# Optimization experiments

Hardware: AMD Instinct MI355X
Metric: run time of the kernel (lower is better)

Reference implementation:

```python
import jax, jax.numpy as jnp
import numpy as np

D_MODEL = 512
NUM_HEADS = 8
D_K = D_MODEL // NUM_HEADS  # 64, also d_v
SEQ_LEN = 4096


def setup_inputs() -> dict:
    key = jax.random.key(0)
    k1, k2, k3, k4, k5 = jax.random.split(key, 5)
    scale = jnp.float32(1.0 / np.sqrt(D_MODEL))  # keep exp(scores) finite
    return {
        "embeded_seq": jax.random.normal(k1, (SEQ_LEN, D_MODEL), jnp.float32),
        "q_proj": jax.random.normal(k2, (NUM_HEADS, D_MODEL, D_K), jnp.float32) * scale,
        "k_proj": jax.random.normal(k3, (NUM_HEADS, D_MODEL, D_K), jnp.float32) * scale,
        "v_proj": jax.random.normal(k4, (NUM_HEADS, D_MODEL, D_K), jnp.float32) * scale,
        "out_proj": jax.random.normal(k5, (NUM_HEADS * D_K, D_MODEL), jnp.float32) * scale,
    }


def reference(embeded_seq, q_proj, k_proj, v_proj, out_proj):
    # Per-head linear projections: (S, D) x (H, D, d_k) -> (H, S, d_k)
    qs = jnp.einsum("sd,hdk->hsk", embeded_seq, q_proj)
    ks = jnp.einsum("sd,hdk->hsk", embeded_seq, k_proj)
    vs = jnp.einsum("sd,hdv->hsv", embeded_seq, v_proj)

    # Scores: (H, S, S), scaled by sqrt(d_k)
    scores = jnp.einsum("hsk,htk->hst", qs, ks) / jnp.float32(np.sqrt(D_K))

    # Faithful to the original: torch.sum(e_powered) is a GLOBAL scalar sum
    # over all heads and positions (a buggy "softmax"), not a row softmax.
    e = jnp.exp(scores)
    softmaxed = e / jnp.sum(e)

    # Attention output per head: (H, S, d_v)
    head_attns = jnp.einsum("hst,htv->hsv", softmaxed, vs)

    # Concat heads along feature dim -> (S, H*d_v), then output projection
    concat = jnp.transpose(head_attns, (1, 0, 2)).reshape(SEQ_LEN, NUM_HEADS * D_K)
    return concat @ out_proj
```

## Files before the change

kernel.cpp:

```cpp
#include <hip/hip_runtime.h>
#include <stdint.h>

#define S_LEN 4096
#define DMODEL 512
#define NHEAD 8
#define DK 64
#define SPLIT 4
#define TBLK 64
#define NT ((S_LEN / SPLIT) / TBLK)

typedef __attribute__((ext_vector_type(8))) short short8;
typedef __attribute__((ext_vector_type(4))) float f32x4;
typedef __attribute__((ext_vector_type(16))) float f32x16;
typedef __attribute__((ext_vector_type(4))) unsigned int uint4v;
typedef __attribute__((ext_vector_type(2))) unsigned long long ull2;

__device__ __forceinline__ unsigned short f2bf(float f) {
    unsigned int u = __float_as_uint(f);
    u = (u + 0x7fffu + ((u >> 16) & 1u)) >> 16;
    return (unsigned short)u;
}

__device__ __forceinline__ void gload16(const unsigned short* g, unsigned short* l) {
    __builtin_amdgcn_global_load_lds(
        (const __attribute__((address_space(1))) unsigned int*)g,
        (__attribute__((address_space(3))) unsigned int*)l, 16, 0, 0);
}


__global__ void cast_bf16_kernel(const float* __restrict__ in,
                                 unsigned short* __restrict__ out, int n4,
                                 float* __restrict__ Z) {
    int i = blockIdx.x * blockDim.x + threadIdx.x;
    if (i == 0) *Z = 0.0f;
    if (i >= n4) return;
    float4 v = reinterpret_cast<const float4*>(in)[i];
    ushort4 o;
    o.x = f2bf(v.x); o.y = f2bf(v.y); o.z = f2bf(v.z); o.w = f2bf(v.w);
    reinterpret_cast<ushort4*>(out)[i] = o;
}

__global__ __launch_bounds__(256) void transpose_qkv_kernel(
    const float* __restrict__ wq, const float* __restrict__ wk, const float* __restrict__ wv,
    unsigned short* __restrict__ oq, unsigned short* __restrict__ ok, unsigned short* __restrict__ ov) {
    __shared__ float tile[64][65];
    const int p = blockIdx.y >> 3, h = blockIdx.y & 7;
    const int r0 = blockIdx.x * 64;
    const float* in = ((p == 0) ? wq : (p == 1) ? wk : wv) + (size_t)h * DMODEL * DK;
    unsigned short* out = ((p == 0) ? oq : (p == 1) ? ok : ov) + (size_t)h * DK * DMODEL;
    const int tr = threadIdx.x >> 4, tc4 = (threadIdx.x & 15) * 4;
#pragma unroll
    for (int rr = 0; rr < 4; ++rr) {
        float4 v = *reinterpret_cast<const float4*>(in + (size_t)(r0 + tr + rr * 16) * DK + tc4);
        tile[tr + rr * 16][tc4 + 0] = v.x;
        tile[tr + rr * 16][tc4 + 1] = v.y;
        tile[tr + rr * 16][tc4 + 2] = v.z;
        tile[tr + rr * 16][tc4 + 3] = v.w;
    }
    __syncthreads();
#pragma unroll
    for (int rr = 0; rr < 4; ++rr) {
        const int c = tr + rr * 16;
        ushort4 o;
        o.x = f2bf(tile[tc4 + 0][c]);
        o.y = f2bf(tile[tc4 + 1][c]);
        o.z = f2bf(tile[tc4 + 2][c]);
        o.w = f2bf(tile[tc4 + 3][c]);
        *reinterpret_cast<ushort4*>(out + (size_t)c * DMODEL + r0 + tc4) = o;
    }
}

__global__ __launch_bounds__(256) void transpose_wo_kernel(
    const float* __restrict__ in, unsigned short* __restrict__ out) {
    __shared__ float tile[64][65];
    const int c0 = blockIdx.x * 64, r0 = blockIdx.y * 64;
    const int tr = threadIdx.x >> 4, tc4 = (threadIdx.x & 15) * 4;
#pragma unroll
    for (int rr = 0; rr < 4; ++rr) {
        float4 v = *reinterpret_cast<const float4*>(in + (size_t)(r0 + tr + rr * 16) * DMODEL + c0 + tc4);
        tile[tr + rr * 16][tc4 + 0] = v.x;
        tile[tr + rr * 16][tc4 + 1] = v.y;
        tile[tr + rr * 16][tc4 + 2] = v.z;
        tile[tr + rr * 16][tc4 + 3] = v.w;
    }
    __syncthreads();
#pragma unroll
    for (int rr = 0; rr < 4; ++rr) {
        const int c = tr + rr * 16;
        ushort4 o;
        o.x = f2bf(tile[tc4 + 0][c]);
        o.y = f2bf(tile[tc4 + 1][c]);
        o.z = f2bf(tile[tc4 + 2][c]);
        o.w = f2bf(tile[tc4 + 3][c]);
        *reinterpret_cast<ushort4*>(out + (size_t)(c0 + c) * DMODEL + r0 + tc4) = o;
    }
}

__global__ __launch_bounds__(256, 2) void proj_tiled_kernel(
    const unsigned short* __restrict__ A,
    const unsigned short* __restrict__ BTall,
    unsigned short* __restrict__ Qo,
    unsigned short* __restrict__ Ko,
    unsigned short* __restrict__ Vo) {
    __shared__ unsigned short lds[32768];
    const int tid = threadIdx.x;
    const int w = tid >> 6, l = tid & 63;
    const int l15 = l & 15, lg = l >> 4;
    const int wr = w >> 1, wc = w & 1;
    const int m0 = blockIdx.x * 128, n0 = blockIdx.y * 128;
    const int srow = l >> 3;
    const int schk = ((l & 7) ^ srow) << 3;
    f32x4 acc[4][4] = {};
    {
        unsigned short* ab = &lds[0];
        unsigned short* bb = &lds[8192];
#pragma unroll
        for (int g = 0; g < 4; ++g) {
            gload16(A + (size_t)(m0 + w * 32 + g * 8 + srow) * DMODEL + schk,
                    ab + (w * 32 + g * 8) * 64);
            gload16(BTall + (size_t)(n0 + w * 32 + g * 8 + srow) * DMODEL + schk,
                    bb + (w * 32 + g * 8) * 64);
        }
    }
    __syncthreads();
    for (int kt = 0; kt < 8; ++kt) {
        const int b = (kt & 1) * 16384;
        if (kt + 1 < 8) {
            const int nb = ((kt + 1) & 1) * 16384;
            const int k0 = (kt + 1) * 64;
            unsigned short* ab = &lds[nb];
            unsigned short* bb = &lds[nb + 8192];
#pragma unroll
            for (int g = 0; g < 4; ++g) {
                gload16(A + (size_t)(m0 + w * 32 + g * 8 + srow) * DMODEL + k0 + schk,
                        ab + (w * 32 + g * 8) * 64);
                gload16(BTall + (size_t)(n0 + w * 32 + g * 8 + srow) * DMODEL + k0 + schk,
                        bb + (w * 32 + g * 8) * 64);
            }
        }
#pragma unroll
        for (int kk = 0; kk < 2; ++kk) {
            short8 am[4], bn[4];
#pragma unroll
            for (int mi = 0; mi < 4; ++mi) {
                const int row = wr * 64 + mi * 16 + l15;
                am[mi] = *reinterpret_cast<const short8*>(
                    &lds[b + row * 64 + ((kk * 32 + lg * 8) ^ ((row & 7) << 3))]);
            }
#pragma unroll
            for (int ni = 0; ni < 4; ++ni) {
                const int row = wc * 64 + ni * 16 + l15;
                bn[ni] = *reinterpret_cast<const short8*>(
                    &lds[b + 8192 + row * 64 + ((kk * 32 + lg * 8) ^ ((row & 7) << 3))]);
            }
#pragma unroll
            for (int mi = 0; mi < 4; ++mi)
#pragma unroll
                for (int ni = 0; ni < 4; ++ni)
                    acc[mi][ni] = __builtin_amdgcn_mfma_f32_16x16x32_bf16(am[mi], bn[ni], acc[mi][ni], 0, 0, 0);
        }
        __syncthreads();
    }
#pragma unroll
    for (int ni = 0; ni < 4; ++ni) {
        const int n = n0 + wc * 64 + ni * 16;
        const int p = n >> 9, h = (n >> 6) & 7, vb = n & 63;
        unsigned short* dst = ((p == 0) ? Qo : (p == 1) ? Ko : Vo) + (size_t)h * S_LEN * DK;
        const float sc = (p == 0) ? 0.125f : 1.0f;
#pragma unroll
        for (int mi = 0; mi < 4; ++mi) {
            const int s = m0 + wr * 64 + mi * 16 + lg * 4;
#pragma unroll
            for (int r = 0; r < 4; ++r)
                dst[(size_t)(s + r) * DK + vb + l15] = f2bf(acc[mi][ni][r] * sc);
        }
    }
}

__global__ __launch_bounds__(256, 2) void out_tiled_kernel(
    const unsigned short* __restrict__ A,
    const unsigned short* __restrict__ BT,
    const float* __restrict__ Z,
    float* __restrict__ Cout) {
    __shared__ unsigned short lds[32768];
    const int tid = threadIdx.x;
    const int w = tid >> 6, l = tid & 63;
    const int l15 = l & 15, lg = l >> 4;
    const int wr = w >> 1, wc = w & 1;
    const int m0 = blockIdx.x * 128, n0 = blockIdx.y * 128;
    const int srow = l >> 3;
    const int schk = ((l & 7) ^ srow) << 3;
    const float invZ = 1.0f / *Z;
    f32x4 acc[4][4] = {};
    {
        unsigned short* ab = &lds[0];
        unsigned short* bb = &lds[8192];
#pragma unroll
        for (int g = 0; g < 4; ++g) {
            gload16(A + (size_t)(m0 + w * 32 + g * 8 + srow) * DMODEL + schk,
                    ab + (w * 32 + g * 8) * 64);
            gload16(BT + (size_t)(n0 + w * 32 + g * 8 + srow) * DMODEL + schk,
                    bb + (w * 32 + g * 8) * 64);
        }
    }
    __syncthreads();
    for (int kt = 0; kt < 8; ++kt) {
        const int b = (kt & 1) * 16384;
        if (kt + 1 < 8) {
            const int nb = ((kt + 1) & 1) * 16384;
            const int k0 = (kt + 1) * 64;
            unsigned short* ab = &lds[nb];
            unsigned short* bb = &lds[nb + 8192];
#pragma unroll
            for (int g = 0; g < 4; ++g) {
                gload16(A + (size_t)(m0 + w * 32 + g * 8 + srow) * DMODEL + k0 + schk,
                        ab + (w * 32 + g * 8) * 64);
                gload16(BT + (size_t)(n0 + w * 32 + g * 8 + srow) * DMODEL + k0 + schk,
                        bb + (w * 32 + g * 8) * 64);
            }
        }
#pragma unroll
        for (int kk = 0; kk < 2; ++kk) {
            short8 am[4], bn[4];
#pragma unroll
            for (int mi = 0; mi < 4; ++mi) {
                const int row = wr * 64 + mi * 16 + l15;
                am[mi] = *reinterpret_cast<const short8*>(
                    &lds[b + row * 64 + ((kk * 32 + lg * 8) ^ ((row & 7) << 3))]);
            }
#pragma unroll
            for (int ni = 0; ni < 4; ++ni) {
                const int row = wc * 64 + ni * 16 + l15;
                bn[ni] = *reinterpret_cast<const short8*>(
                    &lds[b + 8192 + row * 64 + ((kk * 32 + lg * 8) ^ ((row & 7) << 3))]);
            }
#pragma unroll
            for (int mi = 0; mi < 4; ++mi)
#pragma unroll
                for (int ni = 0; ni < 4; ++ni)
                    acc[mi][ni] = __builtin_amdgcn_mfma_f32_16x16x32_bf16(am[mi], bn[ni], acc[mi][ni], 0, 0, 0);
        }
        __syncthreads();
    }
#pragma unroll
    for (int ni = 0; ni < 4; ++ni) {
        const int n = n0 + wc * 64 + ni * 16;
#pragma unroll
        for (int mi = 0; mi < 4; ++mi) {
            const int s = m0 + wr * 64 + mi * 16 + lg * 4;
#pragma unroll
            for (int r = 0; r < 4; ++r)
                Cout[(size_t)(s + r) * DMODEL + n + l15] = acc[mi][ni][r] * invZ;
        }
    }
}

__global__ __launch_bounds__(256) void vt_kernel(const unsigned short* __restrict__ Vb,
                                                 unsigned short* __restrict__ VT) {
    __shared__ unsigned short tile[4096];
    int h = blockIdx.y, t0 = blockIdx.x * 64;
    const unsigned short* Vh = Vb + h * (S_LEN * DK);
    unsigned short* VTh = VT + h * (DK * S_LEN);
    int c8 = (threadIdx.x & 7) * 8, rw = threadIdx.x >> 3;
#pragma unroll
    for (int rr = 0; rr < 2; ++rr) {
        int t = rw + rr * 32;
        short8 v = *reinterpret_cast<const short8*>(Vh + (t0 + t) * DK + c8);
        *reinterpret_cast<short8*>(&tile[t * 64 + (c8 ^ ((t & 7) << 3))]) = v;
    }
    __syncthreads();
#pragma unroll
    for (int rr = 0; rr < 2; ++rr) {
        int v = rw + rr * 32;
        short8 s;
#pragma unroll
        for (int i = 0; i < 8; ++i) {
            int t = c8 + i;
            s[i] = (short)tile[t * 64 + (v ^ ((t & 7) << 3))];
        }
        *reinterpret_cast<short8*>(VTh + v * S_LEN + t0 + c8) = s;
    }
}

__device__ __forceinline__ void make_pfrag(const f32x16& s, short8 pf[2],
                                           float& z0, float& z1) {
    float p[16];
#pragma unroll
    for (int r = 0; r < 16; ++r) p[r] = __expf(s[r]);
#pragma unroll
    for (int r = 0; r < 16; r += 2) { z0 += p[r]; z1 += p[r + 1]; }
    unsigned int c[8];
#pragma unroll
    for (int j = 0; j < 8; ++j)
        asm("v_cvt_pk_bf16_f32 %0, %1, %2" : "=v"(c[j]) : "v"(p[2 * j]), "v"(p[2 * j + 1]));
    uint4v wa = {c[0], c[1], c[2], c[3]};
    uint4v wb = {c[4], c[5], c[6], c[7]};
    pf[0] = __builtin_bit_cast(short8, wa);
    pf[1] = __builtin_bit_cast(short8, wb);
}

__global__ __launch_bounds__(256, 2) void attn_kernel(
    const unsigned short* __restrict__ Qg,
    const unsigned short* __restrict__ Kg,
    const unsigned short* __restrict__ VTg,
    float* __restrict__ Opart,
    float* __restrict__ Z) {
    __shared__ unsigned short lds[32768];
    const int tid = threadIdx.x;
    const int w = tid >> 6, l = tid & 63;
    const int l31 = l & 31, lh = l >> 5;
    const int qb = blockIdx.x, h = blockIdx.y, sp = blockIdx.z;
    const unsigned short* Qh = Qg + h * (S_LEN * DK);
    const unsigned short* Kh = Kg + h * (S_LEN * DK);
    const unsigned short* VTh = VTg + h * (DK * S_LEN);
    const int t_base = sp * (S_LEN / SPLIT);
    const int q0 = qb * 256 + w * 64;

    short8 bq[2][4];
#pragma unroll
    for (int qc = 0; qc < 2; ++qc)
#pragma unroll
        for (int ks = 0; ks < 4; ++ks)
            bq[qc][ks] = *reinterpret_cast<const short8*>(
                Qh + (q0 + qc * 32 + l31) * DK + ks * 16 + lh * 8);

    f32x16 oacc[2][2] = {};
    float z0 = 0.0f, z1 = 0.0f;

    const int srow = l >> 3;
    const int scol = ((l & 7) ^ srow) << 3;
    const unsigned short* gkb = Kh + (size_t)(t_base + w * 16 + srow) * DK + scol;
    const unsigned short* gvb = VTh + (size_t)(w * 16 + srow) * S_LEN + t_base + scol;

    auto stage = [&](int tt) {
        const int boff = (tt & 3) * 8192;
        unsigned short* kb = &lds[boff + w * 1024];
        unsigned short* vb = &lds[boff + 4096 + w * 1024];
        gload16(gkb + (size_t)tt * TBLK * DK, kb);
        gload16(gkb + (size_t)tt * TBLK * DK + 8 * DK, kb + 512);
        gload16(gvb + tt * TBLK, vb);
        gload16(gvb + tt * TBLK + 8 * S_LEN, vb + 512);
    };

    stage(0);
    stage(1);
    for (int it = 0; it < NT; ++it) {
        if (it + 2 < NT) stage(it + 2);
        if (it < NT - 2)       asm volatile("s_waitcnt vmcnt(8)" ::: "memory");
        else if (it == NT - 2) asm volatile("s_waitcnt vmcnt(4)" ::: "memory");
        else                   asm volatile("s_waitcnt vmcnt(0)" ::: "memory");
        __builtin_amdgcn_s_barrier();
        const int b = (it & 3) * 8192;
#pragma unroll
        for (int tc = 0; tc < 2; ++tc) {
            f32x16 s0 = {}, s1 = {};
            const int tA = tc * 32 + l31;
            __builtin_amdgcn_s_setprio(1);
#pragma unroll
            for (int ks = 0; ks < 4; ++ks) {
                short8 ka = *reinterpret_cast<const short8*>(
                    &lds[b + tA * 64 + ((ks * 16 + lh * 8) ^ ((tA & 7) << 3))]);
                s0 = __builtin_amdgcn_mfma_f32_32x32x16_bf16(ka, bq[0][ks], s0, 0, 0, 0);
                s1 = __builtin_amdgcn_mfma_f32_32x32x16_bf16(ka, bq[1][ks], s1, 0, 0, 0);
            }
            __builtin_amdgcn_s_setprio(0);
            short8 pf0[2], pf1[2];
            make_pfrag(s0, pf0, z0, z1);
            make_pfrag(s1, pf1, z0, z1);
            __builtin_amdgcn_s_setprio(1);
#pragma unroll
            for (int sub = 0; sub < 2; ++sub) {
#pragma unroll
                for (int vc = 0; vc < 2; ++vc) {
                    const int vx = l31 & 7;
                    const int cc = tc * 4 + sub * 2;
                    const int base = b + 4096 + (vc * 32 + l31) * 64;
                    unsigned long long d0 = *reinterpret_cast<const unsigned long long*>(
                        &lds[base + ((cc ^ vx) << 3) + lh * 4]);
                    unsigned long long d1 = *reinterpret_cast<const unsigned long long*>(
                        &lds[base + (((cc + 1) ^ vx) << 3) + lh * 4]);
                    ull2 dd = {d0, d1};
                    short8 bv = __builtin_bit_cast(short8, dd);
                    oacc[0][vc] = __builtin_amdgcn_mfma_f32_32x32x16_bf16(pf0[sub], bv, oacc[0][vc], 0, 0, 0);
                    oacc[1][vc] = __builtin_amdgcn_mfma_f32_32x32x16_bf16(pf1[sub], bv, oacc[1][vc], 0, 0, 0);
                }
            }
            __builtin_amdgcn_s_setprio(0);
        }
    }
    float* Op = Opart + ((size_t)(sp * NHEAD + h) * S_LEN + q0) * DK;
#pragma unroll
    for (int qc = 0; qc < 2; ++qc)
#pragma unroll
        for (int vc = 0; vc < 2; ++vc)
#pragma unroll
            for (int reg = 0; reg < 16; ++reg) {
                int q = qc * 32 + (reg & 3) + 8 * (reg >> 2) + 4 * lh;
                Op[(size_t)q * DK + vc * 32 + l31] = oacc[qc][vc][reg];
            }
    float zloc = z0 + z1;
#pragma unroll
    for (int off = 32; off > 0; off >>= 1) zloc += __shfl_xor(zloc, off, 64);
    if (l == 0) atomicAdd(Z, zloc);
}

__global__ __launch_bounds__(256) void reduce_o_kernel(
    const float* __restrict__ Opart, unsigned short* __restrict__ cc) {
    const int HSV = NHEAD * S_LEN * DK;
    int i = blockIdx.x * blockDim.x + threadIdx.x;
    if (i * 4 >= HSV) return;
    f32x4 s = {};
#pragma unroll
    for (int sp = 0; sp < SPLIT; ++sp) {
        f32x4 v = *reinterpret_cast<const f32x4*>(&Opart[(size_t)sp * HSV + i * 4]);
        s += v;
    }
    int e = i * 4;
    int h = e / (S_LEN * DK);
    int rem = e - h * (S_LEN * DK);
    int srow = rem / DK;
    int v = rem - srow * DK;
    ushort4 o4;
    o4.x = f2bf(s[0]); o4.y = f2bf(s[1]); o4.z = f2bf(s[2]); o4.w = f2bf(s[3]);
    *reinterpret_cast<ushort4*>(&cc[srow * DMODEL + h * DK + v]) = o4;
}


extern "C" void kernel_launch(void* const* d_in, const int* in_sizes, int n_in,
                              void* d_out, int out_size, void* d_ws, size_t ws_size,
                              hipStream_t stream) {
    const float* emb = (const float*)d_in[0];
    const float* wq = (const float*)d_in[1];
    const float* wk = (const float*)d_in[2];
    const float* wv = (const float*)d_in[3];
    const float* wo = (const float*)d_in[4];
    float* out = (float*)d_out;
    char* ws = (char*)d_ws;
    unsigned short* embB = (unsigned short*)(ws);
    unsigned short* wqT  = (unsigned short*)(ws + 4194304);
    unsigned short* wkT  = (unsigned short*)(ws + 4718592);
    unsigned short* wvT  = (unsigned short*)(ws + 5242880);
    unsigned short* woT  = (unsigned short*)(ws + 5767168);
    unsigned short* Qb   = (unsigned short*)(ws + 6291456);
    unsigned short* Kb   = (unsigned short*)(ws + 10485760);
    unsigned short* Vb   = (unsigned short*)(ws + 14680064);
    unsigned short* cc   = (unsigned short*)(ws + 18874368);
    float* Z             = (float*)(ws + 23068672);
    float* Opart         = (float*)(ws + 23072768);
    unsigned short* VT   = embB;

    cast_bf16_kernel<<<2048, 256, 0, stream>>>(emb, embB, 524288, Z);
    transpose_qkv_kernel<<<dim3(8, 24), 256, 0, stream>>>(wq, wk, wv, wqT, wkT, wvT);
    transpose_wo_kernel<<<dim3(8, 8), 256, 0, stream>>>(wo, woT);
    proj_tiled_kernel<<<dim3(32, 12), 256, 0, stream>>>(embB, wqT, Qb, Kb, Vb);
    vt_kernel<<<dim3(64, 8), 256, 0, stream>>>(Vb, VT);
    attn_kernel<<<dim3(16, 8, SPLIT), 256, 0, stream>>>(Qb, Kb, VT, Opart, Z);
    reduce_o_kernel<<<2048, 256, 0, stream>>>(Opart, cc);
    out_tiled_kernel<<<dim3(32, 4), 256, 0, stream>>>(cc, woT, Z, out);
}
```

Measured before the change: 105.9 us.

## Software-pipeline attention loop so PV of previous tile overlaps QK/exp of current

Restructures the attention inner loop into a skewed pipeline: QK scores and exp for tile T run while the PV MFMAs consume the probability fragments of tile T-1, with double-buffered P fragments and explicit prologue and epilogue. The aim is to hide the VALU exp/convert latency behind matrix-core work. It also folds log2(e) into the Q scale and uses the native exp2 builtin instead of __expf. The extra live fragments raise register pressure and may affect occupancy under the 2-blocks launch bound.

New measurement: 100.6 us. -5.0%, faster.

```diff
diff --git a/kernel.cpp b/kernel.cpp
--- a/kernel.cpp
+++ b/kernel.cpp
@@ -8,6 +8,14 @@
 #define SPLIT 4
 #define TBLK 64
 #define NT ((S_LEN / SPLIT) / TBLK)
+
+#if __has_builtin(__builtin_amdgcn_exp2f)
+#define EXPFN(x) __builtin_amdgcn_exp2f(x)
+#define QSCALE 0.18033688011112042f
+#else
+#define EXPFN(x) __expf(x)
+#define QSCALE 0.125f
+#endif
 
 typedef __attribute__((ext_vector_type(8))) short short8;
 typedef __attribute__((ext_vector_type(4))) float f32x4;
@@ -166,7 +174,7 @@
         const int n = n0 + wc * 64 + ni * 16;
         const int p = n >> 9, h = (n >> 6) & 7, vb = n & 63;
         unsigned short* dst = ((p == 0) ? Qo : (p == 1) ? Ko : Vo) + (size_t)h * S_LEN * DK;
-        const float sc = (p == 0) ? 0.125f : 1.0f;
+        const float sc = (p == 0) ? QSCALE : 1.0f;
 #pragma unroll
         for (int mi = 0; mi < 4; ++mi) {
             const int s = m0 + wr * 64 + mi * 16 + lg * 4;
@@ -286,7 +294,7 @@
                                            float& z0, float& z1) {
     float p[16];
 #pragma unroll
-    for (int r = 0; r < 16; ++r) p[r] = __expf(s[r]);
+    for (int r = 0; r < 16; ++r) p[r] = EXPFN(s[r]);
 #pragma unroll
     for (int r = 0; r < 16; r += 2) { z0 += p[r]; z1 += p[r + 1]; }
     unsigned int c[8];
@@ -298,6 +306,51 @@
     pf[0] = __builtin_bit_cast(short8, wa);
     pf[1] = __builtin_bit_cast(short8, wb);
 }
+
+#define QK_TC(BC, TC, SD0, SD1)                                                       \
+    {                                                                                 \
+        const int tA_ = (TC) * 32 + l31;                                              \
+        __builtin_amdgcn_s_setprio(1);                                                \
+        _Pragma("unroll") for (int ks_ = 0; ks_ < 4; ++ks_) {                         \
+            short8 ka_ = *reinterpret_cast<const short8*>(                            \
+                &lds[(BC) + tA_ * 64 + ((ks_ * 16 + lh * 8) ^ ((tA_ & 7) << 3))]);    \
+            SD0 = __builtin_amdgcn_mfma_f32_32x32x16_bf16(ka_, bq[0][ks_], SD0, 0, 0, 0); \
+            SD1 = __builtin_amdgcn_mfma_f32_32x32x16_bf16(ka_, bq[1][ks_], SD1, 0, 0, 0); \
+        }                                                                             \
+        __builtin_amdgcn_s_setprio(0);                                                \
+    }
+
+#define PV_HALF(BP, TCP, PFO)                                                         \
+    _Pragma("unroll") for (int sub_ = 0; sub_ < 2; ++sub_)                            \
+    _Pragma("unroll") for (int vc_ = 0; vc_ < 2; ++vc_) {                             \
+        const int cc_ = (TCP) * 4 + sub_ * 2;                                         \
+        const int base_ = (BP) + 4096 + (vc_ * 32 + l31) * 64;                        \
+        unsigned long long d0_ = *reinterpret_cast<const unsigned long long*>(        \
+            &lds[base_ + ((cc_ ^ vx) << 3) + lh * 4]);                                \
+        unsigned long long d1_ = *reinterpret_cast<const unsigned long long*>(        \
+            &lds[base_ + (((cc_ + 1) ^ vx) << 3) + lh * 4]);                          \
+        ull2 dd_ = {d0_, d1_};                                                        \
+        short8 bv_ = __builtin_bit_cast(short8, dd_);                                 \
+        oacc[0][vc_] = __builtin_amdgcn_mfma_f32_32x32x16_bf16(PFO[TCP][0][sub_], bv_, oacc[0][vc_], 0, 0, 0); \
+        oacc[1][vc_] = __builtin_amdgcn_mfma_f32_32x32x16_bf16(PFO[TCP][1][sub_], bv_, oacc[1][vc_], 0, 0, 0); \
+    }
+
+#define STEP_CORE(T, PFN, PFO)                                                        \
+    {                                                                                 \
+        if ((T) + 2 < NT) stage((T) + 2);                                             \
+        const int bC_ = ((T) & 3) * 8192;                                             \
+        const int bP_ = (((T) + 3) & 3) * 8192;                                       \
+        f32x16 sA_ = {}, sB_ = {};                                                    \
+        QK_TC(bC_, 0, sA_, sB_);                                                      \
+        make_pfrag(sA_, PFN[0][0], z0, z1);                                           \
+        PV_HALF(bP_, 0, PFO);                                                         \
+        make_pfrag(sB_, PFN[0][1], z0, z1);                                           \
+        f32x16 sC_ = {}, sD_ = {};                                                    \
+        QK_TC(bC_, 1, sC_, sD_);                                                      \
+        make_pfrag(sC_, PFN[1][0], z0, z1);                                           \
+        PV_HALF(bP_, 1, PFO);                                                         \
+        make_pfrag(sD_, PFN[1][1], z0, z1);                                           \
+    }
 
 __global__ __launch_bounds__(256, 2) void attn_kernel(
     const unsigned short* __restrict__ Qg,
@@ -309,6 +362,7 @@
     const int tid = threadIdx.x;
     const int w = tid >> 6, l = tid & 63;
     const int l31 = l & 31, lh = l >> 5;
+    const int vx = l31 & 7;
     const int qb = blockIdx.x, h = blockIdx.y, sp = blockIdx.z;
     const unsigned short* Qh = Qg + h * (S_LEN * DK);
     const unsigned short* Kh = Kg + h * (S_LEN * DK);
@@ -326,6 +380,7 @@
 
     f32x16 oacc[2][2] = {};
     float z0 = 0.0f, z1 = 0.0f;
+    short8 pfA[2][2][2], pfB[2][2][2];
 
     const int srow = l >> 3;
     const int scol = ((l & 7) ^ srow) << 3;
@@ -344,50 +399,37 @@
 
     stage(0);
     stage(1);
-    for (int it = 0; it < NT; ++it) {
-        if (it + 2 < NT) stage(it + 2);
-        if (it < NT - 2)       asm volatile("s_waitcnt vmcnt(8)" ::: "memory");
-        else if (it == NT - 2) asm volatile("s_waitcnt vmcnt(4)" ::: "memory");
-        else                   asm volatile("s_waitcnt vmcnt(0)" ::: "memory");
+    asm volatile("s_waitcnt vmcnt(4)" ::: "memory");
+    __builtin_amdgcn_s_barrier();
+    {
+        stage(2);
+        f32x16 sA_ = {}, sB_ = {};
+        QK_TC(0, 0, sA_, sB_);
+        make_pfrag(sA_, pfA[0][0], z0, z1);
+        make_pfrag(sB_, pfA[0][1], z0, z1);
+        f32x16 sC_ = {}, sD_ = {};
+        QK_TC(0, 1, sC_, sD_);
+        make_pfrag(sC_, pfA[1][0], z0, z1);
+        make_pfrag(sD_, pfA[1][1], z0, z1);
+    }
+    for (int tp = 0; tp < 7; ++tp) {
+        const int t1 = 2 * tp + 1;
+        asm volatile("s_waitcnt vmcnt(4)" ::: "memory");
         __builtin_amdgcn_s_barrier();
-        const int b = (it & 3) * 8192;
-#pragma unroll
-        for (int tc = 0; tc < 2; ++tc) {
-            f32x16 s0 = {}, s1 = {};
-            const int tA = tc * 32 + l31;
-            __builtin_amdgcn_s_setprio(1);
-#pragma unroll
-            for (int ks = 0; ks < 4; ++ks) {
-                short8 ka = *reinterpret_cast<const short8*>(
-                    &lds[b + tA * 64 + ((ks * 16 + lh * 8) ^ ((tA & 7) << 3))]);
-                s0 = __builtin_amdgcn_mfma_f32_32x32x16_bf16(ka, bq[0][ks], s0, 0, 0, 0);
-                s1 = __builtin_amdgcn_mfma_f32_32x32x16_bf16(ka, bq[1][ks], s1, 0, 0, 0);
-            }
-            __builtin_amdgcn_s_setprio(0);
-            short8 pf0[2], pf1[2];
-            make_pfrag(s0, pf0, z0, z1);
-            make_pfrag(s1, pf1, z0, z1);
-            __builtin_amdgcn_s_setprio(1);
-#pragma unroll
-            for (int sub = 0; sub < 2; ++sub) {
-#pragma unroll
-                for (int vc = 0; vc < 2; ++vc) {
-                    const int vx = l31 & 7;
-                    const int cc = tc * 4 + sub * 2;
-                    const int base = b + 4096 + (vc * 32 + l31) * 64;
-                    unsigned long long d0 = *reinterpret_cast<const unsigned long long*>(
-                        &lds[base + ((cc ^ vx) << 3) + lh * 4]);
-                    unsigned long long d1 = *reinterpret_cast<const unsigned long long*>(
-                        &lds[base + (((cc + 1) ^ vx) << 3) + lh * 4]);
-                    ull2 dd = {d0, d1};
-                    short8 bv = __builtin_bit_cast(short8, dd);
-                    oacc[0][vc] = __builtin_amdgcn_mfma_f32_32x32x16_bf16(pf0[sub], bv, oacc[0][vc], 0, 0, 0);
-                    oacc[1][vc] = __builtin_amdgcn_mfma_f32_32x32x16_bf16(pf1[sub], bv, oacc[1][vc], 0, 0, 0);
-                }
-            }
-            __builtin_amdgcn_s_setprio(0);
-        }
-    }
+        STEP_CORE(t1, pfB, pfA);
+        asm volatile("s_waitcnt vmcnt(4)" ::: "memory");
+        __builtin_amdgcn_s_barrier();
+        STEP_CORE(t1 + 1, pfA, pfB);
+    }
+    asm volatile("s_waitcnt vmcnt(0)" ::: "memory");
+    __builtin_amdgcn_s_barrier();
+    STEP_CORE(15, pfB, pfA);
+    {
+        const int bP_ = (15 & 3) * 8192;
+        PV_HALF(bP_, 0, pfB);
+        PV_HALF(bP_, 1, pfB);
+    }
+
     float* Op = Opart + ((size_t)(sp * NHEAD + h) * S_LEN + q0) * DK;
 #pragma unroll
     for (int qc = 0; qc < 2; ++qc)
```

## Use 512-thread attention blocks with one query tile per wave and exp2

Applied to the files above, without the earlier changes.

The attention kernel now runs 8 waves per block, each owning 32 query rows instead of 64. This halves per-wave accumulator and Q registers so more waves can be resident. The K/V pipeline shrinks from a 4-deep async buffer with waitcnt tuning to a double buffer with a __syncthreads per tile. Separately, the Q scale folds in log2(e) so the kernel can call the hardware exp2 instead of __expf. The trade-off is more block-wide barriers and less prefetch depth, and K/V reuse in registers per wave drops because each K fragment now feeds one query tile instead of two.

Result: slower. 129.2 us (+22.1%).

```diff
diff --git a/kernel.cpp b/kernel.cpp
--- a/kernel.cpp
+++ b/kernel.cpp
@@ -8,6 +8,14 @@
 #define SPLIT 4
 #define TBLK 64
 #define NT ((S_LEN / SPLIT) / TBLK)
+
+#if __has_builtin(__builtin_amdgcn_exp2f)
+#define EXPFN(x) __builtin_amdgcn_exp2f(x)
+#define QSCALE 0.18033688011112042f
+#else
+#define EXPFN(x) __expf(x)
+#define QSCALE 0.125f
+#endif
 
 typedef __attribute__((ext_vector_type(8))) short short8;
 typedef __attribute__((ext_vector_type(4))) float f32x4;
@@ -166,7 +174,7 @@
         const int n = n0 + wc * 64 + ni * 16;
         const int p = n >> 9, h = (n >> 6) & 7, vb = n & 63;
         unsigned short* dst = ((p == 0) ? Qo : (p == 1) ? Ko : Vo) + (size_t)h * S_LEN * DK;
-        const float sc = (p == 0) ? 0.125f : 1.0f;
+        const float sc = (p == 0) ? QSCALE : 1.0f;
 #pragma unroll
         for (int mi = 0; mi < 4; ++mi) {
             const int s = m0 + wr * 64 + mi * 16 + lg * 4;
@@ -286,7 +294,7 @@
                                            float& z0, float& z1) {
     float p[16];
 #pragma unroll
-    for (int r = 0; r < 16; ++r) p[r] = __expf(s[r]);
+    for (int r = 0; r < 16; ++r) p[r] = EXPFN(s[r]);
 #pragma unroll
     for (int r = 0; r < 16; r += 2) { z0 += p[r]; z1 += p[r + 1]; }
     unsigned int c[8];
@@ -299,80 +307,68 @@
     pf[1] = __builtin_bit_cast(short8, wb);
 }
 
-__global__ __launch_bounds__(256, 2) void attn_kernel(
+__global__ __launch_bounds__(512, 4) void attn_kernel(
     const unsigned short* __restrict__ Qg,
     const unsigned short* __restrict__ Kg,
     const unsigned short* __restrict__ VTg,
     float* __restrict__ Opart,
     float* __restrict__ Z) {
-    __shared__ unsigned short lds[32768];
+    __shared__ unsigned short lds[16384];
     const int tid = threadIdx.x;
     const int w = tid >> 6, l = tid & 63;
     const int l31 = l & 31, lh = l >> 5;
+    const int vx = l31 & 7;
     const int qb = blockIdx.x, h = blockIdx.y, sp = blockIdx.z;
     const unsigned short* Qh = Qg + h * (S_LEN * DK);
     const unsigned short* Kh = Kg + h * (S_LEN * DK);
     const unsigned short* VTh = VTg + h * (DK * S_LEN);
     const int t_base = sp * (S_LEN / SPLIT);
-    const int q0 = qb * 256 + w * 64;
-
-    short8 bq[2][4];
-#pragma unroll
-    for (int qc = 0; qc < 2; ++qc)
-#pragma unroll
-        for (int ks = 0; ks < 4; ++ks)
-            bq[qc][ks] = *reinterpret_cast<const short8*>(
-                Qh + (q0 + qc * 32 + l31) * DK + ks * 16 + lh * 8);
-
-    f32x16 oacc[2][2] = {};
+    const int q0 = qb * 256 + w * 32;
+
+    short8 bq[4];
+#pragma unroll
+    for (int ks = 0; ks < 4; ++ks)
+        bq[ks] = *reinterpret_cast<const short8*>(
+            Qh + (q0 + l31) * DK + ks * 16 + lh * 8);
+
+    f32x16 oacc[2] = {};
     float z0 = 0.0f, z1 = 0.0f;
 
     const int srow = l >> 3;
     const int scol = ((l & 7) ^ srow) << 3;
-    const unsigned short* gkb = Kh + (size_t)(t_base + w * 16 + srow) * DK + scol;
-    const unsigned short* gvb = VTh + (size_t)(w * 16 + srow) * S_LEN + t_base + scol;
+    const unsigned short* gkb = Kh + (size_t)(t_base + w * 8 + srow) * DK + scol;
+    const unsigned short* gvb = VTh + (size_t)(w * 8 + srow) * S_LEN + t_base + scol;
 
     auto stage = [&](int tt) {
-        const int boff = (tt & 3) * 8192;
-        unsigned short* kb = &lds[boff + w * 1024];
-        unsigned short* vb = &lds[boff + 4096 + w * 1024];
-        gload16(gkb + (size_t)tt * TBLK * DK, kb);
-        gload16(gkb + (size_t)tt * TBLK * DK + 8 * DK, kb + 512);
-        gload16(gvb + tt * TBLK, vb);
-        gload16(gvb + tt * TBLK + 8 * S_LEN, vb + 512);
+        const int boff = (tt & 1) * 8192;
+        gload16(gkb + (size_t)tt * TBLK * DK, &lds[boff + w * 512]);
+        gload16(gvb + tt * TBLK, &lds[boff + 4096 + w * 512]);
     };
 
     stage(0);
-    stage(1);
+    __syncthreads();
     for (int it = 0; it < NT; ++it) {
-        if (it + 2 < NT) stage(it + 2);
-        if (it < NT - 2)       asm volatile("s_waitcnt vmcnt(8)" ::: "memory");
-        else if (it == NT - 2) asm volatile("s_waitcnt vmcnt(4)" ::: "memory");
-        else                   asm volatile("s_waitcnt vmcnt(0)" ::: "memory");
-        __builtin_amdgcn_s_barrier();
-        const int b = (it & 3) * 8192;
+        const int b = (it & 1) * 8192;
+        if (it + 1 < NT) stage(it + 1);
 #pragma unroll
         for (int tc = 0; tc < 2; ++tc) {
-            f32x16 s0 = {}, s1 = {};
+            f32x16 s = {};
             const int tA = tc * 32 + l31;
             __builtin_amdgcn_s_setprio(1);
 #pragma unroll
             for (int ks = 0; ks < 4; ++ks) {
                 short8 ka = *reinterpret_cast<const short8*>(
                     &lds[b + tA * 64 + ((ks * 16 + lh * 8) ^ ((tA & 7) << 3))]);
-                s0 = __builtin_amdgcn_mfma_f32_32x32x16_bf16(ka, bq[0][ks], s0, 0, 0, 0);
-                s1 = __builtin_amdgcn_mfma_f32_32x32x16_bf16(ka, bq[1][ks], s1, 0, 0, 0);
+                s = __builtin_amdgcn_mfma_f32_32x32x16_bf16(ka, bq[ks], s, 0, 0, 0);
             }
             __builtin_amdgcn_s_setprio(0);
-            short8 pf0[2], pf1[2];
-            make_pfrag(s0, pf0, z0, z1);
-            make_pfrag(s1, pf1, z0, z1);
+            short8 pf[2];
+            make_pfrag(s, pf, z0, z1);
             __builtin_amdgcn_s_setprio(1);
 #pragma unroll
             for (int sub = 0; sub < 2; ++sub) {
 #pragma unroll
                 for (int vc = 0; vc < 2; ++vc) {
-                    const int vx = l31 & 7;
                     const int cc = tc * 4 + sub * 2;
                     const int base = b + 4096 + (vc * 32 + l31) * 64;
                     unsigned long long d0 = *reinterpret_cast<const unsigned long long*>(
@@ -381,23 +377,22 @@
                         &lds[base + (((cc + 1) ^ vx) << 3) + lh * 4]);
                     ull2 dd = {d0, d1};
                     short8 bv = __builtin_bit_cast(short8, dd);
-                    oacc[0][vc] = __builtin_amdgcn_mfma_f32_32x32x16_bf16(pf0[sub], bv, oacc[0][vc], 0, 0, 0);
-                    oacc[1][vc] = __builtin_amdgcn_mfma_f32_32x32x16_bf16(pf1[sub], bv, oacc[1][vc], 0, 0, 0);
+                    oacc[vc] = __builtin_amdgcn_mfma_f32_32x32x16_bf16(pf[sub], bv, oacc[vc], 0, 0, 0);
                 }
             }
             __builtin_amdgcn_s_setprio(0);
         }
-    }
+        __syncthreads();
+    }
+
     float* Op = Opart + ((size_t)(sp * NHEAD + h) * S_LEN + q0) * DK;
 #pragma unroll
-    for (int qc = 0; qc < 2; ++qc)
-#pragma unroll
-        for (int vc = 0; vc < 2; ++vc)
-#pragma unroll
-            for (int reg = 0; reg < 16; ++reg) {
-                int q = qc * 32 + (reg & 3) + 8 * (reg >> 2) + 4 * lh;
-                Op[(size_t)q * DK + vc * 32 + l31] = oacc[qc][vc][reg];
-            }
+    for (int vc = 0; vc < 2; ++vc)
+#pragma unroll
+        for (int reg = 0; reg < 16; ++reg) {
+            int q = (reg & 3) + 8 * (reg >> 2) + 4 * lh;
+            Op[(size_t)q * DK + vc * 32 + l31] = oacc[vc][reg];
+        }
     float zloc = z0 + z1;
 #pragma unroll
     for (int off = 32; off > 0; off >>= 1) zloc += __shfl_xor(zloc, off, 64);
@@ -454,7 +449,7 @@
     transpose_wo_kernel<<<dim3(8, 8), 256, 0, stream>>>(wo, woT);
     proj_tiled_kernel<<<dim3(32, 12), 256, 0, stream>>>(embB, wqT, Qb, Kb, Vb);
     vt_kernel<<<dim3(64, 8), 256, 0, stream>>>(Vb, VT);
-    attn_kernel<<<dim3(16, 8, SPLIT), 256, 0, stream>>>(Qb, Kb, VT, Opart, Z);
+    attn_kernel<<<dim3(16, 8, SPLIT), 512, 0, stream>>>(Qb, Kb, VT, Opart, Z);
     reduce_o_kernel<<<2048, 256, 0, stream>>>(Opart, cc);
     out_tiled_kernel<<<dim3(32, 4), 256, 0, stream>>>(cc, woT, Z, out);
 }
```

## Double the attention split, shrink LDS to double-buffer, store bf16 partials, use exp2

Applied to the files above, without the earlier changes.

Raises the key-split factor from 4 to 8 and halves attention LDS by moving from a 4-deep async ring to a 2-deep double buffer with a full barrier per tile. Launch bounds now allow 4 blocks per CU, which should give more parallelism and occupancy. Partial outputs are stored as bf16 rather than fp32, halving partial-buffer traffic into the reduce kernel. The scale log2(e)/8 is folded into Q so a raw exp2 can replace expf. Costs: shallower prefetch and an extra sync per tile, plus bf16 rounding of the partial sums before reduction.

After: 195.6 us. 1.85x slower.

```diff
diff --git a/kernel.cpp b/kernel.cpp
--- a/kernel.cpp
+++ b/kernel.cpp
@@ -5,9 +5,17 @@
 #define DMODEL 512
 #define NHEAD 8
 #define DK 64
-#define SPLIT 4
+#define SPLIT 8
 #define TBLK 64
 #define NT ((S_LEN / SPLIT) / TBLK)
+
+#if __has_builtin(__builtin_amdgcn_exp2f)
+#define EXPFN(x) __builtin_amdgcn_exp2f(x)
+#define QSCALE 0.18033688011112042f
+#else
+#define EXPFN(x) __expf(x)
+#define QSCALE 0.125f
+#endif
 
 typedef __attribute__((ext_vector_type(8))) short short8;
 typedef __attribute__((ext_vector_type(4))) float f32x4;
@@ -166,7 +174,7 @@
         const int n = n0 + wc * 64 + ni * 16;
         const int p = n >> 9, h = (n >> 6) & 7, vb = n & 63;
         unsigned short* dst = ((p == 0) ? Qo : (p == 1) ? Ko : Vo) + (size_t)h * S_LEN * DK;
-        const float sc = (p == 0) ? 0.125f : 1.0f;
+        const float sc = (p == 0) ? QSCALE : 1.0f;
 #pragma unroll
         for (int mi = 0; mi < 4; ++mi) {
             const int s = m0 + wr * 64 + mi * 16 + lg * 4;
@@ -286,7 +294,7 @@
                                            float& z0, float& z1) {
     float p[16];
 #pragma unroll
-    for (int r = 0; r < 16; ++r) p[r] = __expf(s[r]);
+    for (int r = 0; r < 16; ++r) p[r] = EXPFN(s[r]);
 #pragma unroll
     for (int r = 0; r < 16; r += 2) { z0 += p[r]; z1 += p[r + 1]; }
     unsigned int c[8];
@@ -299,16 +307,17 @@
     pf[1] = __builtin_bit_cast(short8, wb);
 }
 
-__global__ __launch_bounds__(256, 2) void attn_kernel(
+__global__ __launch_bounds__(256, 4) void attn_kernel(
     const unsigned short* __restrict__ Qg,
     const unsigned short* __restrict__ Kg,
     const unsigned short* __restrict__ VTg,
-    float* __restrict__ Opart,
+    unsigned short* __restrict__ Opart,
     float* __restrict__ Z) {
-    __shared__ unsigned short lds[32768];
+    __shared__ unsigned short lds[16384];
     const int tid = threadIdx.x;
     const int w = tid >> 6, l = tid & 63;
     const int l31 = l & 31, lh = l >> 5;
+    const int vx = l31 & 7;
     const int qb = blockIdx.x, h = blockIdx.y, sp = blockIdx.z;
     const unsigned short* Qh = Qg + h * (S_LEN * DK);
     const unsigned short* Kh = Kg + h * (S_LEN * DK);
@@ -329,28 +338,33 @@
 
     const int srow = l >> 3;
     const int scol = ((l & 7) ^ srow) << 3;
-    const unsigned short* gkb = Kh + (size_t)(t_base + w * 16 + srow) * DK + scol;
-    const unsigned short* gvb = VTh + (size_t)(w * 16 + srow) * S_LEN + t_base + scol;
-
-    auto stage = [&](int tt) {
-        const int boff = (tt & 3) * 8192;
-        unsigned short* kb = &lds[boff + w * 1024];
-        unsigned short* vb = &lds[boff + 4096 + w * 1024];
-        gload16(gkb + (size_t)tt * TBLK * DK, kb);
-        gload16(gkb + (size_t)tt * TBLK * DK + 8 * DK, kb + 512);
-        gload16(gvb + tt * TBLK, vb);
-        gload16(gvb + tt * TBLK + 8 * S_LEN, vb + 512);
-    };
-
-    stage(0);
-    stage(1);
+    const unsigned short* gk = Kh + (size_t)(t_base + w * 16 + srow) * DK + scol;
+    const unsigned short* gv0 = VTh + (size_t)(w * 16 + srow) * S_LEN + t_base + scol;
+    const unsigned short* gv1 = gv0 + 8 * S_LEN;
+
+    {
+        unsigned short* kb = &lds[w * 1024];
+        gload16(gk, kb);
+        gload16(gk + 512, kb + 512);
+        unsigned short* vb = &lds[4096 + w * 1024];
+        gload16(gv0, vb);
+        gload16(gv1, vb + 512);
+        gk += 64 * DK; gv0 += 64; gv1 += 64;
+    }
+    __syncthreads();
+
     for (int it = 0; it < NT; ++it) {
-        if (it + 2 < NT) stage(it + 2);
-        if (it < NT - 2)       asm volatile("s_waitcnt vmcnt(8)" ::: "memory");
-        else if (it == NT - 2) asm volatile("s_waitcnt vmcnt(4)" ::: "memory");
-        else                   asm volatile("s_waitcnt vmcnt(0)" ::: "memory");
-        __builtin_amdgcn_s_barrier();
-        const int b = (it & 3) * 8192;
+        const int b = (it & 1) * 8192;
+        if (it + 1 < NT) {
+            const int nb = ((it + 1) & 1) * 8192;
+            unsigned short* kb = &lds[nb + w * 1024];
+            gload16(gk, kb);
+            gload16(gk + 512, kb + 512);
+            unsigned short* vb = &lds[nb + 4096 + w * 1024];
+            gload16(gv0, vb);
+            gload16(gv1, vb + 512);
+            gk += 64 * DK; gv0 += 64; gv1 += 64;
+        }
 #pragma unroll
         for (int tc = 0; tc < 2; ++tc) {
             f32x16 s0 = {}, s1 = {};
@@ -372,7 +386,6 @@
             for (int sub = 0; sub < 2; ++sub) {
 #pragma unroll
                 for (int vc = 0; vc < 2; ++vc) {
-                    const int vx = l31 & 7;
                     const int cc = tc * 4 + sub * 2;
                     const int base = b + 4096 + (vc * 32 + l31) * 64;
                     unsigned long long d0 = *reinterpret_cast<const unsigned long long*>(
@@ -387,8 +400,9 @@
             }
             __builtin_amdgcn_s_setprio(0);
         }
-    }
-    float* Op = Opart + ((size_t)(sp * NHEAD + h) * S_LEN + q0) * DK;
+        __syncthreads();
+    }
+    unsigned short* Op = Opart + ((size_t)(sp * NHEAD + h) * S_LEN + q0) * DK;
 #pragma unroll
     for (int qc = 0; qc < 2; ++qc)
 #pragma unroll
@@ -396,7 +410,7 @@
 #pragma unroll
             for (int reg = 0; reg < 16; ++reg) {
                 int q = qc * 32 + (reg & 3) + 8 * (reg >> 2) + 4 * lh;
-                Op[(size_t)q * DK + vc * 32 + l31] = oacc[qc][vc][reg];
+                Op[(size_t)q * DK + vc * 32 + l31] = f2bf(oacc[qc][vc][reg]);
             }
     float zloc = z0 + z1;
 #pragma unroll
@@ -405,15 +419,18 @@
 }
 
 __global__ __launch_bounds__(256) void reduce_o_kernel(
-    const float* __restrict__ Opart, unsigned short* __restrict__ cc) {
+    const unsigned short* __restrict__ Opart, unsigned short* __restrict__ cc) {
     const int HSV = NHEAD * S_LEN * DK;
     int i = blockIdx.x * blockDim.x + threadIdx.x;
     if (i * 4 >= HSV) return;
-    f32x4 s = {};
+    float s0 = 0, s1 = 0, s2 = 0, s3 = 0;
 #pragma unroll
     for (int sp = 0; sp < SPLIT; ++sp) {
-        f32x4 v = *reinterpret_cast<const f32x4*>(&Opart[(size_t)sp * HSV + i * 4]);
-        s += v;
+        ushort4 v = *reinterpret_cast<const ushort4*>(&Opart[(size_t)sp * HSV + i * 4]);
+        s0 += __uint_as_float((unsigned int)v.x << 16);
+        s1 += __uint_as_float((unsigned int)v.y << 16);
+        s2 += __uint_as_float((unsigned int)v.z << 16);
+        s3 += __uint_as_float((unsigned int)v.w << 16);
     }
     int e = i * 4;
     int h = e / (S_LEN * DK);
@@ -421,7 +438,7 @@
     int srow = rem / DK;
     int v = rem - srow * DK;
     ushort4 o4;
-    o4.x = f2bf(s[0]); o4.y = f2bf(s[1]); o4.z = f2bf(s[2]); o4.w = f2bf(s[3]);
+    o4.x = f2bf(s0); o4.y = f2bf(s1); o4.z = f2bf(s2); o4.w = f2bf(s3);
     *reinterpret_cast<ushort4*>(&cc[srow * DMODEL + h * DK + v]) = o4;
 }
 
@@ -446,7 +463,7 @@
     unsigned short* Vb   = (unsigned short*)(ws + 14680064);
     unsigned short* cc   = (unsigned short*)(ws + 18874368);
     float* Z             = (float*)(ws + 23068672);
-    float* Opart         = (float*)(ws + 23072768);
+    unsigned short* Opart = (unsigned short*)(ws + 23072768);
     unsigned short* VT   = embB;
 
     cast_bf16_kernel<<<2048, 256, 0, stream>>>(emb, embB, 524288, Z);
```
